# Performance work log

Measured on AMD Instinct MI355X. Metric: run time of the kernel, lower is better.

Reference implementation:

```python
import jax, jax.numpy as jnp
import numpy as np

N, D_IN, D_BLOCK, D_OUT, E, K = 65536, 128, 256, 128, 8, 2


def setup_inputs() -> dict:
    key = jax.random.key(0)
    ks = jax.random.split(key, 8)
    s_in = 1.0 / np.sqrt(D_IN)
    s_h = 1.0 / np.sqrt(D_BLOCK)
    return {
        "x": jax.random.normal(ks[0], (N, D_IN), jnp.float32),
        "Wg": jax.random.normal(ks[1], (D_IN, E), jnp.float32) * s_in,
        "W1": jax.random.normal(ks[2], (E, D_IN, D_BLOCK), jnp.float32) * s_in,
        "b1": jax.random.normal(ks[3], (E, D_BLOCK), jnp.float32) * 0.01,
        "W2": jax.random.normal(ks[4], (E, D_BLOCK, D_BLOCK), jnp.float32) * s_h,
        "b2": jax.random.normal(ks[5], (E, D_BLOCK), jnp.float32) * 0.01,
        "Wo": jax.random.normal(ks[6], (D_BLOCK, D_OUT), jnp.float32) * s_h,
        "bo": jax.random.normal(ks[7], (D_OUT,), jnp.float32) * 0.01,
    }


def reference(x, Wg, W1, b1, W2, b2, Wo, bo):
    # Router: linear gate -> top-k -> softmax over the k selected logits,
    # scattered back to a dense [N, E] combine-weight matrix (zeros elsewhere).
    logits = x @ Wg                                   # [N, E]
    topv, topi = jax.lax.top_k(logits, K)             # [N, K]
    w_topk = jax.nn.softmax(topv, axis=-1)            # [N, K]
    onehot = jax.nn.one_hot(topi, E, dtype=x.dtype)   # [N, K, E]
    weights = jnp.einsum("nk,nke->ne", w_topk, onehot)  # [N, E]

    # Expert MLPs (n_blocks=2, ReLU, dropout=0 at eval), computed for all
    # experts over all tokens; unselected experts have weight 0, so the
    # weighted combine reproduces the original masked gather/scatter math.
    h = jax.nn.relu(jnp.einsum("nd,edh->enh", x, W1) + b1[:, None, :])   # [E,N,H]
    h = jax.nn.relu(jnp.einsum("enh,ehg->eng", h, W2) + b2[:, None, :])  # [E,N,H]
    y = jnp.einsum("enh,ho->eno", h, Wo) + bo                             # [E,N,O]

    # Weighted scatter-add combine: outs[n] = sum_e weights[n,e] * y[e,n]
    return jnp.einsum("ne,eno->no", weights, y)
```

## Files before the change

### kernel.cpp

```cpp
#include <hip/hip_runtime.h>
#include <math.h>

typedef unsigned short ushort_t;
typedef __attribute__((ext_vector_type(8))) short bf16x8;
typedef __attribute__((ext_vector_type(4))) float f32x4;
typedef __attribute__((ext_vector_type(8))) unsigned short u16x8;

#define N_TOK 65536
#define DIN 128
#define HD 256
#define DOUT 128
#define NEXP 8
#define MT 32
#define NSEG 32
#define SEGCAP 2048
#define SEGTILES (SEGCAP / MT)

#define G_INIT 8192
#define G_ROUTER 2048
#define G_PACK 400

__device__ __forceinline__ unsigned short f2bf(float f) {
    union { float f; unsigned int i; } v; v.f = f;
    unsigned int i = v.i;
    return (unsigned short)((i + 0x7FFFu + ((i >> 16) & 1u)) >> 16);
}

#define RT_TPB 32
__global__ __launch_bounds__(256)
void prep_kernel(const float* __restrict__ x,
                 const float* __restrict__ Wg,
                 const float* __restrict__ W1,
                 const float* __restrict__ W2,
                 const float* __restrict__ Wo,
                 const float* __restrict__ bo,
                 int* __restrict__ segcnt,
                 int* __restrict__ list_tok,
                 float* __restrict__ list_w,
                 ushort_t* __restrict__ wt1f,
                 ushort_t* __restrict__ wt2f,
                 ushort_t* __restrict__ wotf,
                 float* __restrict__ out) {
    int tid = threadIdx.x;
    int bx = blockIdx.x;

    if (bx < G_INIT) {
        int gid = bx * 256 + tid;
        float4 b = ((const float4*)bo)[gid & 31];
        ((float4*)out)[gid] = b;
        return;
    }
    if (bx < G_INIT + G_ROUTER) {
        int rb = bx - G_INIT;
        __shared__ float wgsT[NEXP * 132];
        __shared__ int lcnt[NEXP];
        __shared__ int lbase[NEXP];
        if (tid < NEXP) lcnt[tid] = 0;
        for (int i = tid; i < DIN * NEXP; i += 256) {
            int e = i & 7, k = i >> 3;
            wgsT[e * 132 + k] = Wg[i];
        }
        __syncthreads();

        int s = tid & 7;
        int tl = tid >> 3;
        int n = rb * RT_TPB + tl;

        const float4* xr = (const float4*)(x + (size_t)n * DIN + s * 16);
        float4 xv[4];
#pragma unroll
        for (int j = 0; j < 4; j++) xv[j] = xr[j];

        float lg[NEXP];
#pragma unroll
        for (int e = 0; e < NEXP; e++) {
            const float4* wp = (const float4*)(wgsT + e * 132 + s * 16);
            float a = 0.f;
#pragma unroll
            for (int j = 0; j < 4; j++) {
                float4 wv = wp[j];
                a += xv[j].x * wv.x + xv[j].y * wv.y + xv[j].z * wv.z + xv[j].w * wv.w;
            }
            lg[e] = a;
        }
#pragma unroll
        for (int d = 1; d < 8; d <<= 1) {
#pragma unroll
            for (int e = 0; e < NEXP; e++) lg[e] += __shfl_xor(lg[e], d, 64);
        }
        int e0 = 0; float v0 = lg[0];
#pragma unroll
        for (int e = 1; e < NEXP; e++) if (lg[e] > v0) { v0 = lg[e]; e0 = e; }
        int e1 = -1; float v1 = -3.0e38f;
#pragma unroll
        for (int e = 0; e < NEXP; e++) if (e != e0 && lg[e] > v1) { v1 = lg[e]; e1 = e; }
        float t = expf(v1 - v0);
        float inv = 1.0f / (1.0f + t);
        float w0 = inv, w1 = t * inv;

        bool writer = (s == 0);
        int p0 = 0, p1 = 0;
        if (writer) {
            p0 = atomicAdd(&lcnt[e0], 1);
            p1 = atomicAdd(&lcnt[e1], 1);
        }
        __syncthreads();
        int c = rb & (NSEG - 1);
        if (tid < NEXP) lbase[tid] = atomicAdd(&segcnt[tid * NSEG + c], lcnt[tid]);
        __syncthreads();
        if (writer) {
            int q0 = lbase[e0] + p0;
            int idx0 = (e0 * NSEG + c) * SEGCAP + q0;
            list_tok[idx0] = n;
            list_w[idx0] = w0;
            int q1 = lbase[e1] + p1;
            int idx1 = (e1 * NSEG + c) * SEGCAP + q1;
            list_tok[idx1] = n;
            list_w[idx1] = w1;
        }
        return;
    }
    int id = (bx - G_INIT - G_ROUTER) * 256 + tid;
    const float* src; ushort_t* dst; int Nn, ksteps, c;
    if (id < 32768) {
        int e = id >> 12; c = id & 4095;
        Nn = HD; ksteps = 4; src = W1 + (size_t)e * DIN * HD; dst = wt1f + (size_t)id * 8;
    } else if (id < 98304) {
        int t2 = id - 32768; int e = t2 >> 13; c = t2 & 8191;
        Nn = HD; ksteps = 8; src = W2 + (size_t)e * HD * HD; dst = wt2f + (size_t)t2 * 8;
    } else {
        int t2 = id - 98304; c = t2;
        Nn = DOUT; ksteps = 8; src = Wo; dst = wotf + (size_t)t2 * 8;
    }
    int L = c & 63; int kc = c >> 6;
    int kstep = kc % ksteps; int ntile = kc / ksteps;
    int q = L >> 4, m = L & 15;
    int n = ntile * 16 + m; int k0 = kstep * 32 + q * 8;
    u16x8 v;
#pragma unroll
    for (int j = 0; j < 8; j++) v[j] = f2bf(src[(size_t)(k0 + j) * Nn + n]);
    *(u16x8*)dst = v;
}

__global__ __launch_bounds__(256, 6)
void expert_kernel(const float* __restrict__ x,
                   const int* __restrict__ segcnt,
                   const int* __restrict__ list_tok,
                   const float* __restrict__ list_w,
                   const ushort_t* __restrict__ wt1f,
                   const ushort_t* __restrict__ wt2f,
                   const ushort_t* __restrict__ wotf,
                   const float* __restrict__ b1,
                   const float* __restrict__ b2,
                   float* __restrict__ out) {
    int bid = blockIdx.x;
    int e = bid & 7;
    int c = (bid >> 3) & (NSEG - 1);
    int t = bid >> 8;
    int cnt = segcnt[e * NSEG + c];
    int base = t * MT;
    if (base >= cnt) return;
    int rows = cnt - base; if (rows > MT) rows = MT;
    int lidx = (e * NSEG + c) * SEGCAP + base;

    __shared__ __align__(16) ushort_t bufA[4096];
    __shared__ __align__(16) ushort_t bufH[8192];
    __shared__ int toks_s[MT];
    __shared__ float wts_s[MT];

    int tid = threadIdx.x;
    int lane = tid & 63;
    int w = tid >> 6;
    int q = lane >> 4;
    int mcol = lane & 15;

    if (tid < MT) {
        int rr = tid < rows ? tid : rows - 1;
        toks_s[tid] = list_tok[lidx + rr];
        wts_s[tid] = list_w[lidx + rr];
    }
    for (int cc = tid; cc < 512; cc += 256) {
        int row = cc >> 4;
        int kchunk = cc & 15;
        int rr = row < rows ? row : rows - 1;
        int tok = list_tok[lidx + rr];
        const float4* src = (const float4*)(x + (size_t)tok * DIN + kchunk * 8);
        float4 lo = src[0], hi = src[1];
        u16x8 v;
        v[0] = f2bf(lo.x); v[1] = f2bf(lo.y); v[2] = f2bf(lo.z); v[3] = f2bf(lo.w);
        v[4] = f2bf(hi.x); v[5] = f2bf(hi.y); v[6] = f2bf(hi.z); v[7] = f2bf(hi.w);
        int kstep = kchunk >> 2, qq = kchunk & 3;
        int dchunk = (kstep * 2 + (row >> 4)) * 64 + qq * 16 + (row & 15);
        ((u16x8*)bufA)[dchunk] = v;
    }
    __syncthreads();

    const bf16x8* Albs = (const bf16x8*)bufA;
    const bf16x8* Hlbs = (const bf16x8*)bufH;

    f32x4 acc[2][4];
#pragma unroll
    for (int mt = 0; mt < 2; mt++)
#pragma unroll
        for (int nt = 0; nt < 4; nt++) acc[mt][nt] = (f32x4){0.f, 0.f, 0.f, 0.f};
    const bf16x8* B1 = (const bf16x8*)(wt1f + (size_t)e * 4096 * 8);
#pragma unroll
    for (int kstep = 0; kstep < 4; kstep++) {
        bf16x8 a[2];
#pragma unroll
        for (int mt = 0; mt < 2; mt++) a[mt] = Albs[(kstep * 2 + mt) * 64 + lane];
#pragma unroll
        for (int nt = 0; nt < 4; nt++) {
            bf16x8 b = B1[((w * 4 + nt) * 4 + kstep) * 64 + lane];
#pragma unroll
            for (int mt = 0; mt < 2; mt++)
                acc[mt][nt] = __builtin_amdgcn_mfma_f32_16x16x32_bf16(a[mt], b, acc[mt][nt], 0, 0, 0);
        }
    }
#pragma unroll
    for (int nt = 0; nt < 4; nt++) {
        int nn = (w * 4 + nt) * 16 + mcol;
        float bias = b1[e * HD + nn];
        int kstep = nn >> 5, qq = (nn >> 3) & 3, jj = nn & 7;
#pragma unroll
        for (int mt = 0; mt < 2; mt++) {
#pragma unroll
            for (int r = 0; r < 4; r++) {
                float v = acc[mt][nt][r] + bias;
                v = v > 0.f ? v : 0.f;
                int chunk = (kstep * 2 + mt) * 64 + qq * 16 + q * 4 + r;
                bufH[chunk * 8 + jj] = f2bf(v);
            }
        }
    }
    __syncthreads();

    f32x4 acc2[2][4];
#pragma unroll
    for (int mt = 0; mt < 2; mt++)
#pragma unroll
        for (int nt = 0; nt < 4; nt++) acc2[mt][nt] = (f32x4){0.f, 0.f, 0.f, 0.f};
    const bf16x8* B2 = (const bf16x8*)(wt2f + (size_t)e * 8192 * 8);
#pragma unroll
    for (int kstep = 0; kstep < 8; kstep++) {
        bf16x8 a[2];
#pragma unroll
        for (int mt = 0; mt < 2; mt++) a[mt] = Hlbs[(kstep * 2 + mt) * 64 + lane];
#pragma unroll
        for (int nt = 0; nt < 4; nt++) {
            bf16x8 b = B2[((w * 4 + nt) * 8 + kstep) * 64 + lane];
#pragma unroll
            for (int mt = 0; mt < 2; mt++)
                acc2[mt][nt] = __builtin_amdgcn_mfma_f32_16x16x32_bf16(a[mt], b, acc2[mt][nt], 0, 0, 0);
        }
    }
    __syncthreads();
#pragma unroll
    for (int nt = 0; nt < 4; nt++) {
        int nn = (w * 4 + nt) * 16 + mcol;
        float bias = b2[e * HD + nn];
        int kstep = nn >> 5, qq = (nn >> 3) & 3, jj = nn & 7;
#pragma unroll
        for (int mt = 0; mt < 2; mt++) {
#pragma unroll
            for (int r = 0; r < 4; r++) {
                float v = acc2[mt][nt][r] + bias;
                v = v > 0.f ? v : 0.f;
                int chunk = (kstep * 2 + mt) * 64 + qq * 16 + q * 4 + r;
                bufH[chunk * 8 + jj] = f2bf(v);
            }
        }
    }
    __syncthreads();

    f32x4 acc3[2][2];
#pragma unroll
    for (int mt = 0; mt < 2; mt++)
#pragma unroll
        for (int nt = 0; nt < 2; nt++) acc3[mt][nt] = (f32x4){0.f, 0.f, 0.f, 0.f};
    const bf16x8* B3 = (const bf16x8*)wotf;
#pragma unroll
    for (int kstep = 0; kstep < 8; kstep++) {
        bf16x8 a[2];
#pragma unroll
        for (int mt = 0; mt < 2; mt++) a[mt] = Hlbs[(kstep * 2 + mt) * 64 + lane];
#pragma unroll
        for (int nt = 0; nt < 2; nt++) {
            bf16x8 b = B3[((w * 2 + nt) * 8 + kstep) * 64 + lane];
#pragma unroll
            for (int mt = 0; mt < 2; mt++)
                acc3[mt][nt] = __builtin_amdgcn_mfma_f32_16x16x32_bf16(a[mt], b, acc3[mt][nt], 0, 0, 0);
        }
    }
#pragma unroll
    for (int mt = 0; mt < 2; mt++) {
#pragma unroll
        for (int r = 0; r < 4; r++) {
            int row = mt * 16 + q * 4 + r;
            if (row < rows) {
                int tok = toks_s[row];
                float wgt = wts_s[row];
                float* dst = out + (size_t)tok * DOUT;
#pragma unroll
                for (int nt = 0; nt < 2; nt++) {
                    int col = (w * 2 + nt) * 16 + mcol;
                    atomicAdd(&dst[col], wgt * acc3[mt][nt][r]);
                }
            }
        }
    }
}

extern "C" void kernel_launch(void* const* d_in, const int* in_sizes, int n_in,
                              void* d_out, int out_size, void* d_ws, size_t ws_size,
                              hipStream_t stream) {
    const float* x  = (const float*)d_in[0];
    const float* Wg = (const float*)d_in[1];
    const float* W1 = (const float*)d_in[2];
    const float* b1 = (const float*)d_in[3];
    const float* W2 = (const float*)d_in[4];
    const float* b2 = (const float*)d_in[5];
    const float* Wo = (const float*)d_in[6];
    const float* bo = (const float*)d_in[7];
    float* out = (float*)d_out;

    char* ws = (char*)d_ws;
    size_t off = 0;
    int* segcnt    = (int*)(ws + off);    off += 1024;
    int* list_tok  = (int*)(ws + off);    off += (size_t)NEXP * NSEG * SEGCAP * 4;
    float* list_w  = (float*)(ws + off);  off += (size_t)NEXP * NSEG * SEGCAP * 4;
    ushort_t* wt1f = (ushort_t*)(ws + off); off += (size_t)NEXP * DIN * HD * 2;
    ushort_t* wt2f = (ushort_t*)(ws + off); off += (size_t)NEXP * HD * HD * 2;
    ushort_t* wotf = (ushort_t*)(ws + off); off += (size_t)HD * DOUT * 2;

    hipMemsetAsync(segcnt, 0, 1024, stream);
    prep_kernel<<<G_INIT + G_ROUTER + G_PACK, 256, 0, stream>>>(
        x, Wg, W1, W2, Wo, bo, segcnt, list_tok, list_w, wt1f, wt2f, wotf, out);
    expert_kernel<<<NEXP * NSEG * SEGTILES, 256, 0, stream>>>(
        x, segcnt, list_tok, list_w, wt1f, wt2f, wotf, b1, b2, out);
}
```

Before: 213.3 us.

## Make each wave own 16 rows end-to-end with swizzled private LDS, removing block barriers

Restructures the expert MLP kernel so each wave processes its own 16 token rows across all output columns, using a private LDS slice instead of a block-shared one. This eliminates all __syncthreads between the three GEMM stages and adds an XOR swizzle on LDS chunks to reduce bank conflicts. Tile size grows to 64 rows per block, block index decoding is reordered to group by expert, and the occupancy hint is lowered. In exchange each wave streams all weight fragments itself and holds many more accumulators in registers.

Result: slower. 643.0 us (+201.5%).

```diff
diff --git a/kernel.cpp b/kernel.cpp
--- a/kernel.cpp
+++ b/kernel.cpp
@@ -11,7 +11,7 @@
 #define HD 256
 #define DOUT 128
 #define NEXP 8
-#define MT 32
+#define MT 64
 #define NSEG 32
 #define SEGCAP 2048
 #define SEGTILES (SEGCAP / MT)
@@ -25,6 +25,7 @@
     unsigned int i = v.i;
     return (unsigned short)((i + 0x7FFFu + ((i >> 16) & 1u)) >> 16);
 }
+__device__ __forceinline__ int swz(int chunk) { return chunk ^ ((chunk >> 4) & 7); }
 
 #define RT_TPB 32
 __global__ __launch_bounds__(256)
@@ -142,7 +143,7 @@
     *(u16x8*)dst = v;
 }
 
-__global__ __launch_bounds__(256, 6)
+__global__ __launch_bounds__(256, 4)
 void expert_kernel(const float* __restrict__ x,
                    const int* __restrict__ segcnt,
                    const int* __restrict__ list_tok,
@@ -154,159 +155,120 @@
                    const float* __restrict__ b2,
                    float* __restrict__ out) {
     int bid = blockIdx.x;
-    int e = bid & 7;
-    int c = (bid >> 3) & (NSEG - 1);
-    int t = bid >> 8;
+    int e = bid >> 10;
+    int c = (bid >> 5) & (NSEG - 1);
+    int t = bid & (SEGTILES - 1);
     int cnt = segcnt[e * NSEG + c];
     int base = t * MT;
     if (base >= cnt) return;
     int rows = cnt - base; if (rows > MT) rows = MT;
     int lidx = (e * NSEG + c) * SEGCAP + base;
 
-    __shared__ __align__(16) ushort_t bufA[4096];
-    __shared__ __align__(16) ushort_t bufH[8192];
-    __shared__ int toks_s[MT];
-    __shared__ float wts_s[MT];
+    __shared__ __align__(16) ushort_t bufH[16384];
 
     int tid = threadIdx.x;
     int lane = tid & 63;
     int w = tid >> 6;
     int q = lane >> 4;
     int mcol = lane & 15;
-
-    if (tid < MT) {
-        int rr = tid < rows ? tid : rows - 1;
-        toks_s[tid] = list_tok[lidx + rr];
-        wts_s[tid] = list_w[lidx + rr];
-    }
-    for (int cc = tid; cc < 512; cc += 256) {
-        int row = cc >> 4;
-        int kchunk = cc & 15;
-        int rr = row < rows ? row : rows - 1;
-        int tok = list_tok[lidx + rr];
-        const float4* src = (const float4*)(x + (size_t)tok * DIN + kchunk * 8);
+    int w16 = w * 16;
+    if (w16 >= rows) return;
+    int nr = rows - w16; if (nr > 16) nr = 16;
+
+    ushort_t* hb = bufH + w * 4096;
+    const bf16x8* Hl = (const bf16x8*)hb;
+    const bf16x8* B1 = (const bf16x8*)(wt1f + (size_t)e * 4096 * 8);
+    const bf16x8* B2 = (const bf16x8*)(wt2f + (size_t)e * 8192 * 8);
+    const bf16x8* B3 = (const bf16x8*)wotf;
+
+#pragma unroll
+    for (int it = 0; it < 4; it++) {
+        int m = it * 4 + q;
+        int rr = m < nr ? m : nr - 1;
+        int tok = list_tok[lidx + w16 + rr];
+        const float4* src = (const float4*)(x + (size_t)tok * DIN + mcol * 8);
         float4 lo = src[0], hi = src[1];
         u16x8 v;
         v[0] = f2bf(lo.x); v[1] = f2bf(lo.y); v[2] = f2bf(lo.z); v[3] = f2bf(lo.w);
         v[4] = f2bf(hi.x); v[5] = f2bf(hi.y); v[6] = f2bf(hi.z); v[7] = f2bf(hi.w);
-        int kstep = kchunk >> 2, qq = kchunk & 3;
-        int dchunk = (kstep * 2 + (row >> 4)) * 64 + qq * 16 + (row & 15);
-        ((u16x8*)bufA)[dchunk] = v;
-    }
-    __syncthreads();
-
-    const bf16x8* Albs = (const bf16x8*)bufA;
-    const bf16x8* Hlbs = (const bf16x8*)bufH;
-
-    f32x4 acc[2][4];
-#pragma unroll
-    for (int mt = 0; mt < 2; mt++)
-#pragma unroll
-        for (int nt = 0; nt < 4; nt++) acc[mt][nt] = (f32x4){0.f, 0.f, 0.f, 0.f};
-    const bf16x8* B1 = (const bf16x8*)(wt1f + (size_t)e * 4096 * 8);
+        int chunk = (mcol >> 2) * 64 + (mcol & 3) * 16 + m;
+        ((u16x8*)hb)[swz(chunk)] = v;
+    }
+
+    f32x4 acc[16];
+#pragma unroll
+    for (int nt = 0; nt < 16; nt++) acc[nt] = (f32x4){0.f, 0.f, 0.f, 0.f};
 #pragma unroll
     for (int kstep = 0; kstep < 4; kstep++) {
-        bf16x8 a[2];
-#pragma unroll
-        for (int mt = 0; mt < 2; mt++) a[mt] = Albs[(kstep * 2 + mt) * 64 + lane];
-#pragma unroll
-        for (int nt = 0; nt < 4; nt++) {
-            bf16x8 b = B1[((w * 4 + nt) * 4 + kstep) * 64 + lane];
-#pragma unroll
-            for (int mt = 0; mt < 2; mt++)
-                acc[mt][nt] = __builtin_amdgcn_mfma_f32_16x16x32_bf16(a[mt], b, acc[mt][nt], 0, 0, 0);
-        }
-    }
-#pragma unroll
-    for (int nt = 0; nt < 4; nt++) {
-        int nn = (w * 4 + nt) * 16 + mcol;
+        bf16x8 a = Hl[swz(kstep * 64 + lane)];
+#pragma unroll
+        for (int nt = 0; nt < 16; nt++) {
+            bf16x8 b = B1[(nt * 4 + kstep) * 64 + lane];
+            acc[nt] = __builtin_amdgcn_mfma_f32_16x16x32_bf16(a, b, acc[nt], 0, 0, 0);
+        }
+    }
+#pragma unroll
+    for (int nt = 0; nt < 16; nt++) {
+        int nn = nt * 16 + mcol;
         float bias = b1[e * HD + nn];
-        int kstep = nn >> 5, qq = (nn >> 3) & 3, jj = nn & 7;
-#pragma unroll
-        for (int mt = 0; mt < 2; mt++) {
-#pragma unroll
-            for (int r = 0; r < 4; r++) {
-                float v = acc[mt][nt][r] + bias;
-                v = v > 0.f ? v : 0.f;
-                int chunk = (kstep * 2 + mt) * 64 + qq * 16 + q * 4 + r;
-                bufH[chunk * 8 + jj] = f2bf(v);
-            }
-        }
-    }
-    __syncthreads();
-
-    f32x4 acc2[2][4];
-#pragma unroll
-    for (int mt = 0; mt < 2; mt++)
-#pragma unroll
-        for (int nt = 0; nt < 4; nt++) acc2[mt][nt] = (f32x4){0.f, 0.f, 0.f, 0.f};
-    const bf16x8* B2 = (const bf16x8*)(wt2f + (size_t)e * 8192 * 8);
+        int k2 = nn >> 5, qq = (nn >> 3) & 3, jj = nn & 7;
+#pragma unroll
+        for (int r = 0; r < 4; r++) {
+            float v = acc[nt][r] + bias;
+            v = v > 0.f ? v : 0.f;
+            int chunk = k2 * 64 + qq * 16 + q * 4 + r;
+            hb[swz(chunk) * 8 + jj] = f2bf(v);
+        }
+    }
+
+    f32x4 acc2[16];
+#pragma unroll
+    for (int nt = 0; nt < 16; nt++) acc2[nt] = (f32x4){0.f, 0.f, 0.f, 0.f};
 #pragma unroll
     for (int kstep = 0; kstep < 8; kstep++) {
-        bf16x8 a[2];
-#pragma unroll
-        for (int mt = 0; mt < 2; mt++) a[mt] = Hlbs[(kstep * 2 + mt) * 64 + lane];
-#pragma unroll
-        for (int nt = 0; nt < 4; nt++) {
-            bf16x8 b = B2[((w * 4 + nt) * 8 + kstep) * 64 + lane];
-#pragma unroll
-            for (int mt = 0; mt < 2; mt++)
-                acc2[mt][nt] = __builtin_amdgcn_mfma_f32_16x16x32_bf16(a[mt], b, acc2[mt][nt], 0, 0, 0);
-        }
-    }
-    __syncthreads();
-#pragma unroll
-    for (int nt = 0; nt < 4; nt++) {
-        int nn = (w * 4 + nt) * 16 + mcol;
+        bf16x8 a = Hl[swz(kstep * 64 + lane)];
+#pragma unroll
+        for (int nt = 0; nt < 16; nt++) {
+            bf16x8 b = B2[(nt * 8 + kstep) * 64 + lane];
+            acc2[nt] = __builtin_amdgcn_mfma_f32_16x16x32_bf16(a, b, acc2[nt], 0, 0, 0);
+        }
+    }
+#pragma unroll
+    for (int nt = 0; nt < 16; nt++) {
+        int nn = nt * 16 + mcol;
         float bias = b2[e * HD + nn];
-        int kstep = nn >> 5, qq = (nn >> 3) & 3, jj = nn & 7;
-#pragma unroll
-        for (int mt = 0; mt < 2; mt++) {
-#pragma unroll
-            for (int r = 0; r < 4; r++) {
-                float v = acc2[mt][nt][r] + bias;
-                v = v > 0.f ? v : 0.f;
-                int chunk = (kstep * 2 + mt) * 64 + qq * 16 + q * 4 + r;
-                bufH[chunk * 8 + jj] = f2bf(v);
-            }
-        }
-    }
-    __syncthreads();
-
-    f32x4 acc3[2][2];
-#pragma unroll
-    for (int mt = 0; mt < 2; mt++)
-#pragma unroll
-        for (int nt = 0; nt < 2; nt++) acc3[mt][nt] = (f32x4){0.f, 0.f, 0.f, 0.f};
-    const bf16x8* B3 = (const bf16x8*)wotf;
+        int k2 = nn >> 5, qq = (nn >> 3) & 3, jj = nn & 7;
+#pragma unroll
+        for (int r = 0; r < 4; r++) {
+            float v = acc2[nt][r] + bias;
+            v = v > 0.f ? v : 0.f;
+            int chunk = k2 * 64 + qq * 16 + q * 4 + r;
+            hb[swz(chunk) * 8 + jj] = f2bf(v);
+        }
+    }
+
+    f32x4 acc3[8];
+#pragma unroll
+    for (int nt = 0; nt < 8; nt++) acc3[nt] = (f32x4){0.f, 0.f, 0.f, 0.f};
 #pragma unroll
     for (int kstep = 0; kstep < 8; kstep++) {
-        bf16x8 a[2];
-#pragma unroll
-        for (int mt = 0; mt < 2; mt++) a[mt] = Hlbs[(kstep * 2 + mt) * 64 + lane];
-#pragma unroll
-        for (int nt = 0; nt < 2; nt++) {
-            bf16x8 b = B3[((w * 2 + nt) * 8 + kstep) * 64 + lane];
-#pragma unroll
-            for (int mt = 0; mt < 2; mt++)
-                acc3[mt][nt] = __builtin_amdgcn_mfma_f32_16x16x32_bf16(a[mt], b, acc3[mt][nt], 0, 0, 0);
-        }
-    }
-#pragma unroll
-    for (int mt = 0; mt < 2; mt++) {
-#pragma unroll
-        for (int r = 0; r < 4; r++) {
-            int row = mt * 16 + q * 4 + r;
-            if (row < rows) {
-                int tok = toks_s[row];
-                float wgt = wts_s[row];
-                float* dst = out + (size_t)tok * DOUT;
-#pragma unroll
-                for (int nt = 0; nt < 2; nt++) {
-                    int col = (w * 2 + nt) * 16 + mcol;
-                    atomicAdd(&dst[col], wgt * acc3[mt][nt][r]);
-                }
-            }
+        bf16x8 a = Hl[swz(kstep * 64 + lane)];
+#pragma unroll
+        for (int nt = 0; nt < 8; nt++) {
+            bf16x8 b = B3[(nt * 8 + kstep) * 64 + lane];
+            acc3[nt] = __builtin_amdgcn_mfma_f32_16x16x32_bf16(a, b, acc3[nt], 0, 0, 0);
+        }
+    }
+#pragma unroll
+    for (int r = 0; r < 4; r++) {
+        int grow = w16 + q * 4 + r;
+        if (grow < rows) {
+            int tok = list_tok[lidx + grow];
+            float wgt = list_w[lidx + grow];
+            float* dst = out + (size_t)tok * DOUT;
+#pragma unroll
+            for (int nt = 0; nt < 8; nt++)
+                atomicAdd(&dst[nt * 16 + mcol], wgt * acc3[nt][r]);
         }
     }
 }
```
